# Kernel optimization log

Hardware: AMD Instinct MI355X
Metric: run time of the kernel (lower is better)

The kernel has to match this reference:

```python
import jax, jax.numpy as jnp
import numpy as np

MIN_RES, MAX_RES, NUM_LOD, BAND_WIDTH = 16, 512, 8, 19
CODEBOOK_SIZE = 2 ** BAND_WIDTH  # 524288
_b = np.exp((np.log(MAX_RES) - np.log(MIN_RES)) / (NUM_LOD - 1))
LODS = [int(1 + np.floor(MIN_RES * _b ** l)) for l in range(NUM_LOD)]
SIZES = [min(CODEBOOK_SIZE, r ** 3) for r in LODS]
PRIMES = (1, 2654435761, 805459861)  # Instant-NGP spatial hash primes
N_PTS = 2_000_000

# corner offsets of the unit cube, [8,3]
_OFFS = np.array([[(i >> 2) & 1, (i >> 1) & 1, i & 1] for i in range(8)], dtype=np.int32)


def _hash_interp(p01, table, res, size):
    """Hashed trilinear interpolation for one LOD. p01:[N,3] in [0,1], table:[size]."""
    x = p01 * (res - 1)                                   # [N,3]
    c0 = jnp.clip(jnp.floor(x), 0, res - 2).astype(jnp.int32)
    frac = x - c0.astype(jnp.float32)                     # [N,3]
    offs = jnp.asarray(_OFFS)                             # [8,3]
    corners = (c0[:, None, :] + offs[None]).astype(jnp.uint32)  # [N,8,3]
    h = (corners[..., 0] * jnp.uint32(PRIMES[0])
         ^ corners[..., 1] * jnp.uint32(PRIMES[1])
         ^ corners[..., 2] * jnp.uint32(PRIMES[2]))
    idx = (h % jnp.uint32(size)).astype(jnp.int32)        # [N,8]
    feats = table[idx]                                    # [N,8] gather
    offf = offs.astype(jnp.float32)
    # trilinear weights: prod_d (frac if offset else 1-frac)
    w = jnp.prod(frac[:, None, :] * offf + (1.0 - frac[:, None, :]) * (1.0 - offf), axis=-1)
    return jnp.sum(w * feats, axis=-1)                    # [N]


def setup_inputs() -> dict:
    key = jax.random.key(0)
    k1, k2 = jax.random.split(key)
    pts = jax.random.uniform(k1, (N_PTS, 3), jnp.float32) * 2.0 - 1.0  # [-1,1]^3
    codebook = jax.random.normal(k2, (NUM_LOD, CODEBOOK_SIZE, 1), jnp.float32) * 0.01
    return {"pts": pts, "codebook": codebook}


def reference(pts, codebook):
    p01 = pts / 2.0 + 0.5                                  # normalize to [0,1]
    out = jnp.zeros(pts.shape[0], jnp.float32)
    for i, res in enumerate(LODS):                         # small static loop over LODs
        table = codebook[i, : SIZES[i], 0]                 # static slice -> actual table size
        out = out + _hash_interp(p01, table, res, SIZES[i])
    return out[:, None]                                    # [N, feat_dim=1]
```

## Files before the change

### kernel.cpp

```cpp
#include <hip/hip_runtime.h>
#include <math.h>


static constexpr unsigned CB_STRIDE = 524288u;
static constexpr int WO0 = 0;
static constexpr int WO1 = 4928;
static constexpr int WO2 = 24640;
static constexpr int WO3 = 109824;
static constexpr int WO4 = 467744;
static constexpr int WO5 = 992032;
static constexpr int WO6 = 1516320;
static constexpr int WO7 = 2040608;
static constexpr size_t WS_NEED_BYTES = 2564896u * 2u;

__device__ __forceinline__ unsigned short f32_to_bf16_rne(float f) {
    unsigned u = __float_as_uint(f);
    u = (u + 0x7FFFu + ((u >> 16) & 1u)) >> 16;
    return (unsigned short)u;
}
__device__ __forceinline__ float bf16_to_f32(unsigned short s) {
    return __uint_as_float(((unsigned)s) << 16);
}

template <unsigned SIZE, bool POW2>
__device__ __forceinline__ float lod_interp(float p01x, float p01y, float p01z,
                                            const unsigned short* __restrict__ t,
                                            int res)
{
    const float rm1 = (float)(res - 1);
    float xx = p01x * rm1, yy = p01y * rm1, zz = p01z * rm1;
    const float cmax = (float)(res - 2);
    float fx = fminf(fmaxf(floorf(xx), 0.0f), cmax);
    float fy = fminf(fmaxf(floorf(yy), 0.0f), cmax);
    float fz = fminf(fmaxf(floorf(zz), 0.0f), cmax);
    const float frx = xx - fx, fry = yy - fy, frz = zz - fz;
    const unsigned ix = (unsigned)(int)fx;
    const unsigned iy = (unsigned)(int)fy;
    const unsigned iz = (unsigned)(int)fz;

    const unsigned hx0 = ix;
    const unsigned hx1 = ix + 1u;
    const unsigned hy0 = iy * 2654435761u;
    const unsigned hy1 = hy0 + 2654435761u;
    const unsigned hz0 = iz * 805459861u;
    const unsigned hz1 = hz0 + 805459861u;

    unsigned v0 = hx0 ^ hy0 ^ hz0;
    unsigned v1 = hx0 ^ hy0 ^ hz1;
    unsigned v2 = hx0 ^ hy1 ^ hz0;
    unsigned v3 = hx0 ^ hy1 ^ hz1;
    unsigned v4 = hx1 ^ hy0 ^ hz0;
    unsigned v5 = hx1 ^ hy0 ^ hz1;
    unsigned v6 = hx1 ^ hy1 ^ hz0;
    unsigned v7 = hx1 ^ hy1 ^ hz1;

    if (POW2) {
        const unsigned m = SIZE - 1u;
        v0 &= m; v1 &= m; v2 &= m; v3 &= m; v4 &= m; v5 &= m; v6 &= m; v7 &= m;
    } else {
        v0 %= SIZE; v1 %= SIZE; v2 %= SIZE; v3 %= SIZE;
        v4 %= SIZE; v5 %= SIZE; v6 %= SIZE; v7 %= SIZE;
    }

    const float t000 = bf16_to_f32(t[v0]);
    const float t001 = bf16_to_f32(t[v1]);
    const float t010 = bf16_to_f32(t[v2]);
    const float t011 = bf16_to_f32(t[v3]);
    const float t100 = bf16_to_f32(t[v4]);
    const float t101 = bf16_to_f32(t[v5]);
    const float t110 = bf16_to_f32(t[v6]);
    const float t111 = bf16_to_f32(t[v7]);

    const float wx1 = frx, wx0 = 1.0f - frx;
    const float wy1 = fry, wy0 = 1.0f - fry;
    const float wz1 = frz, wz0 = 1.0f - frz;
    const float w00 = wy0 * wz0, w01 = wy0 * wz1;
    const float w10 = wy1 * wz0, w11 = wy1 * wz1;
    const float sx0 = t000 * w00 + t001 * w01 + t010 * w10 + t011 * w11;
    const float sx1 = t100 * w00 + t101 * w01 + t110 * w10 + t111 * w11;
    return wx0 * sx0 + wx1 * sx1;
}

__global__ __launch_bounds__(1024)
void HashGrid_convert_kernel(const float* __restrict__ codebook,
                             unsigned short* __restrict__ ws)
{
    const int lod = blockIdx.y;
    const int sizes[8] = {4913, 19683, 85184, 357911, 524288, 524288, 524288, 524288};
    const int offs[8]  = {WO0, WO1, WO2, WO3, WO4, WO5, WO6, WO7};
    const int idx = blockIdx.x * 1024 + threadIdx.x;
    if (idx < sizes[lod])
        ws[offs[lod] + idx] = f32_to_bf16_rne(codebook[(unsigned)lod * CB_STRIDE + idx]);
}

__global__ __launch_bounds__(256, 4)
void HashGrid_88278757802387_kernel(const float* __restrict__ pts,
                                    const unsigned short* __restrict__ ws,
                                    float* __restrict__ out,
                                    int n, int res7)
{
    const int i = blockIdx.x * 256 + threadIdx.x;
    if (i >= n) return;

    const float p01x = pts[3 * i + 0] * 0.5f + 0.5f;
    const float p01y = pts[3 * i + 1] * 0.5f + 0.5f;
    const float p01z = pts[3 * i + 2] * 0.5f + 0.5f;

    float acc = 0.0f;
    acc += lod_interp<4913u,   false>(p01x, p01y, p01z, ws + WO0, 17);
    acc += lod_interp<19683u,  false>(p01x, p01y, p01z, ws + WO1, 27);
    acc += lod_interp<85184u,  false>(p01x, p01y, p01z, ws + WO2, 44);
    acc += lod_interp<357911u, false>(p01x, p01y, p01z, ws + WO3, 71);
    acc += lod_interp<524288u, true >(p01x, p01y, p01z, ws + WO4, 116);
    acc += lod_interp<524288u, true >(p01x, p01y, p01z, ws + WO5, 191);
    acc += lod_interp<524288u, true >(p01x, p01y, p01z, ws + WO6, 313);
    acc += lod_interp<524288u, true >(p01x, p01y, p01z, ws + WO7, res7);

    out[i] = acc;
}

__global__ __launch_bounds__(256, 4)
void HashGrid_fallback_kernel(const float* __restrict__ pts,
                              const float* __restrict__ codebook,
                              float* __restrict__ out,
                              int n, int res7)
{
    const int i = blockIdx.x * 256 + threadIdx.x;
    if (i >= n) return;
    const float p01x = pts[3 * i + 0] * 0.5f + 0.5f;
    const float p01y = pts[3 * i + 1] * 0.5f + 0.5f;
    const float p01z = pts[3 * i + 2] * 0.5f + 0.5f;
    float acc = 0.0f;
    const int      reslist[8]  = {17, 27, 44, 71, 116, 191, 313, res7};
    const unsigned sizelist[8] = {4913u, 19683u, 85184u, 357911u, 524288u, 524288u, 524288u, 524288u};
    for (int l = 0; l < 8; ++l) {
        const int res = reslist[l];
        const unsigned size = sizelist[l];
        const float rm1 = (float)(res - 1);
        float xx = p01x * rm1, yy = p01y * rm1, zz = p01z * rm1;
        float fx = fminf(fmaxf(floorf(xx), 0.0f), (float)(res - 2));
        float fy = fminf(fmaxf(floorf(yy), 0.0f), (float)(res - 2));
        float fz = fminf(fmaxf(floorf(zz), 0.0f), (float)(res - 2));
        const float frx = xx - fx, fry = yy - fy, frz = zz - fz;
        const unsigned ix = (unsigned)(int)fx, iy = (unsigned)(int)fy, iz = (unsigned)(int)fz;
        const unsigned hy0 = iy * 2654435761u, hy1 = hy0 + 2654435761u;
        const unsigned hz0 = iz * 805459861u,  hz1 = hz0 + 805459861u;
        const unsigned o0 = (ix ^ hy0 ^ hz0) % size,      o1 = (ix ^ hy0 ^ hz1) % size;
        const unsigned o2 = (ix ^ hy1 ^ hz0) % size,      o3 = (ix ^ hy1 ^ hz1) % size;
        const unsigned o4 = ((ix+1u) ^ hy0 ^ hz0) % size, o5 = ((ix+1u) ^ hy0 ^ hz1) % size;
        const unsigned o6 = ((ix+1u) ^ hy1 ^ hz0) % size, o7 = ((ix+1u) ^ hy1 ^ hz1) % size;
        const float* tab = codebook + (unsigned)l * CB_STRIDE;
        const float wx1 = frx, wx0 = 1.0f - frx;
        const float wy1 = fry, wy0 = 1.0f - fry;
        const float wz1 = frz, wz0 = 1.0f - frz;
        const float w00 = wy0*wz0, w01 = wy0*wz1, w10 = wy1*wz0, w11 = wy1*wz1;
        acc += wx0 * (tab[o0]*w00 + tab[o1]*w01 + tab[o2]*w10 + tab[o3]*w11)
             + wx1 * (tab[o4]*w00 + tab[o5]*w01 + tab[o6]*w10 + tab[o7]*w11);
    }
    out[i] = acc;
}

extern "C" void kernel_launch(void* const* d_in, const int* in_sizes, int n_in,
                              void* d_out, int out_size, void* d_ws, size_t ws_size,
                              hipStream_t stream)
{
    const float* pts      = (const float*)d_in[0];
    const float* codebook = (const float*)d_in[1];
    float* out            = (float*)d_out;
    const int n = in_sizes[0] / 3;

    const double b = exp((log(512.0) - log(16.0)) / 7.0);
    const int res7 = (int)(1.0 + floor(16.0 * pow(b, 7.0)));

    const bool use_ws = (d_ws != nullptr) && (ws_size >= WS_NEED_BYTES);
    const int blocks = (n + 255) / 256;

    if (use_ws) {
        unsigned short* ws = (unsigned short*)d_ws;
        hipLaunchKernelGGL(HashGrid_convert_kernel, dim3(512, 8), dim3(1024),
                           0, stream, codebook, ws);
        hipLaunchKernelGGL(HashGrid_88278757802387_kernel, dim3(blocks), dim3(256),
                           0, stream, pts, ws, out, n, res7);
    } else {
        hipLaunchKernelGGL(HashGrid_fallback_kernel, dim3(blocks), dim3(256),
                           0, stream, pts, codebook, out, n, res7);
    }
}
```

Before: 430.8 us.

## Pipeline hash-table gathers through LDS with global_load_lds and explicit vmcnt waits

Replaces the per-LOD direct gathers with asynchronous global_load_lds dword loads into per-wave LDS slots. Four LODs are kept in flight and consumed with manual s_waitcnt vmcnt counters, issuing the next LOD as each slot drains; bf16 halves are selected from the loaded dword by parity. Point loads and the output store become nontemporal. The aim is to raise memory-level parallelism and hide gather latency, at the cost of 32KB of LDS per block, which may limit occupancy, and fragile hand-counted waits.

```diff
diff --git a/kernel.cpp b/kernel.cpp
--- a/kernel.cpp
+++ b/kernel.cpp
@@ -3,14 +3,14 @@
 
 
 static constexpr unsigned CB_STRIDE = 524288u;
-static constexpr int WO0 = 0;
-static constexpr int WO1 = 4928;
-static constexpr int WO2 = 24640;
-static constexpr int WO3 = 109824;
-static constexpr int WO4 = 467744;
-static constexpr int WO5 = 992032;
-static constexpr int WO6 = 1516320;
-static constexpr int WO7 = 2040608;
+static constexpr unsigned WO0 = 0;
+static constexpr unsigned WO1 = 4928;
+static constexpr unsigned WO2 = 24640;
+static constexpr unsigned WO3 = 109824;
+static constexpr unsigned WO4 = 467744;
+static constexpr unsigned WO5 = 992032;
+static constexpr unsigned WO6 = 1516320;
+static constexpr unsigned WO7 = 2040608;
 static constexpr size_t WS_NEED_BYTES = 2564896u * 2u;
 
 __device__ __forceinline__ unsigned short f32_to_bf16_rne(float f) {
@@ -18,14 +18,29 @@
     u = (u + 0x7FFFu + ((u >> 16) & 1u)) >> 16;
     return (unsigned short)u;
 }
-__device__ __forceinline__ float bf16_to_f32(unsigned short s) {
-    return __uint_as_float(((unsigned)s) << 16);
-}
+
+#define TO_GLB(p) ((const __attribute__((address_space(1))) void*)(p))
+#define TO_LDS(p) ((__attribute__((address_space(3))) void*)(p))
+
+__device__ __forceinline__ void gld(const unsigned short* ws, unsigned elem,
+                                    unsigned* lds_dst)
+{
+    const char* g = (const char*)ws + ((elem * 2u) & ~3u);
+    __builtin_amdgcn_global_load_lds(TO_GLB(g), TO_LDS(lds_dst), 4, 0, 0);
+}
+
+#define VMWAIT(N) do { \
+    asm volatile("s_waitcnt vmcnt(" #N ")" ::: "memory"); \
+    __builtin_amdgcn_sched_barrier(0); \
+} while (0)
+
+struct LodState { unsigned selm; float fx, fy, fz; };
 
 template <unsigned SIZE, bool POW2>
-__device__ __forceinline__ float lod_interp(float p01x, float p01y, float p01z,
-                                            const unsigned short* __restrict__ t,
-                                            int res)
+__device__ __forceinline__ LodState issue_lod(float p01x, float p01y, float p01z,
+                                              int res, unsigned wo,
+                                              const unsigned short* __restrict__ ws,
+                                              unsigned* slot )
 {
     const float rm1 = (float)(res - 1);
     float xx = p01x * rm1, yy = p01y * rm1, zz = p01z * rm1;
@@ -33,7 +48,8 @@
     float fx = fminf(fmaxf(floorf(xx), 0.0f), cmax);
     float fy = fminf(fmaxf(floorf(yy), 0.0f), cmax);
     float fz = fminf(fmaxf(floorf(zz), 0.0f), cmax);
-    const float frx = xx - fx, fry = yy - fy, frz = zz - fz;
+    LodState st;
+    st.fx = xx - fx; st.fy = yy - fy; st.fz = zz - fz;
     const unsigned ix = (unsigned)(int)fx;
     const unsigned iy = (unsigned)(int)fy;
     const unsigned iz = (unsigned)(int)fz;
@@ -62,18 +78,50 @@
         v4 %= SIZE; v5 %= SIZE; v6 %= SIZE; v7 %= SIZE;
     }
 
-    const float t000 = bf16_to_f32(t[v0]);
-    const float t001 = bf16_to_f32(t[v1]);
-    const float t010 = bf16_to_f32(t[v2]);
-    const float t011 = bf16_to_f32(t[v3]);
-    const float t100 = bf16_to_f32(t[v4]);
-    const float t101 = bf16_to_f32(t[v5]);
-    const float t110 = bf16_to_f32(t[v6]);
-    const float t111 = bf16_to_f32(t[v7]);
-
-    const float wx1 = frx, wx0 = 1.0f - frx;
-    const float wy1 = fry, wy0 = 1.0f - fry;
-    const float wz1 = frz, wz0 = 1.0f - frz;
+    st.selm = ((wo + v0) & 1u)        | (((wo + v1) & 1u) << 1)
+            | (((wo + v2) & 1u) << 2) | (((wo + v3) & 1u) << 3)
+            | (((wo + v4) & 1u) << 4) | (((wo + v5) & 1u) << 5)
+            | (((wo + v6) & 1u) << 6) | (((wo + v7) & 1u) << 7);
+
+    gld(ws, wo + v0, slot + 0 * 64);
+    gld(ws, wo + v1, slot + 1 * 64);
+    gld(ws, wo + v2, slot + 2 * 64);
+    gld(ws, wo + v3, slot + 3 * 64);
+    gld(ws, wo + v4, slot + 4 * 64);
+    gld(ws, wo + v5, slot + 5 * 64);
+    gld(ws, wo + v6, slot + 6 * 64);
+    gld(ws, wo + v7, slot + 7 * 64);
+    return st;
+}
+
+__device__ __forceinline__ float pick(unsigned d, unsigned sel) {
+    return __uint_as_float(sel ? (d & 0xffff0000u) : (d << 16));
+}
+
+__device__ __forceinline__ float consume_slot(const unsigned* slot, int lane,
+                                              const LodState& st)
+{
+    const unsigned d0 = slot[0 * 64 + lane];
+    const unsigned d1 = slot[1 * 64 + lane];
+    const unsigned d2 = slot[2 * 64 + lane];
+    const unsigned d3 = slot[3 * 64 + lane];
+    const unsigned d4 = slot[4 * 64 + lane];
+    const unsigned d5 = slot[5 * 64 + lane];
+    const unsigned d6 = slot[6 * 64 + lane];
+    const unsigned d7 = slot[7 * 64 + lane];
+
+    const float t000 = pick(d0, (st.selm >> 0) & 1u);
+    const float t001 = pick(d1, (st.selm >> 1) & 1u);
+    const float t010 = pick(d2, (st.selm >> 2) & 1u);
+    const float t011 = pick(d3, (st.selm >> 3) & 1u);
+    const float t100 = pick(d4, (st.selm >> 4) & 1u);
+    const float t101 = pick(d5, (st.selm >> 5) & 1u);
+    const float t110 = pick(d6, (st.selm >> 6) & 1u);
+    const float t111 = pick(d7, (st.selm >> 7) & 1u);
+
+    const float wx1 = st.fx, wx0 = 1.0f - st.fx;
+    const float wy1 = st.fy, wy0 = 1.0f - st.fy;
+    const float wz1 = st.fz, wz0 = 1.0f - st.fz;
     const float w00 = wy0 * wz0, w01 = wy0 * wz1;
     const float w10 = wy1 * wz0, w11 = wy1 * wz1;
     const float sx0 = t000 * w00 + t001 * w01 + t010 * w10 + t011 * w11;
@@ -87,7 +135,7 @@
 {
     const int lod = blockIdx.y;
     const int sizes[8] = {4913, 19683, 85184, 357911, 524288, 524288, 524288, 524288};
-    const int offs[8]  = {WO0, WO1, WO2, WO3, WO4, WO5, WO6, WO7};
+    const unsigned offs[8] = {WO0, WO1, WO2, WO3, WO4, WO5, WO6, WO7};
     const int idx = blockIdx.x * 1024 + threadIdx.x;
     if (idx < sizes[lod])
         ws[offs[lod] + idx] = f32_to_bf16_rne(codebook[(unsigned)lod * CB_STRIDE + idx]);
@@ -99,24 +147,52 @@
                                     float* __restrict__ out,
                                     int n, int res7)
 {
+    __shared__ unsigned lbuf[4][4][8][64];
+    const int w    = threadIdx.x >> 6;
+    const int lane = threadIdx.x & 63;
+    unsigned* s0 = &lbuf[w][0][0][0];
+    unsigned* s1 = &lbuf[w][1][0][0];
+    unsigned* s2 = &lbuf[w][2][0][0];
+    unsigned* s3 = &lbuf[w][3][0][0];
+
     const int i = blockIdx.x * 256 + threadIdx.x;
     if (i >= n) return;
 
-    const float p01x = pts[3 * i + 0] * 0.5f + 0.5f;
-    const float p01y = pts[3 * i + 1] * 0.5f + 0.5f;
-    const float p01z = pts[3 * i + 2] * 0.5f + 0.5f;
-
-    float acc = 0.0f;
-    acc += lod_interp<4913u,   false>(p01x, p01y, p01z, ws + WO0, 17);
-    acc += lod_interp<19683u,  false>(p01x, p01y, p01z, ws + WO1, 27);
-    acc += lod_interp<85184u,  false>(p01x, p01y, p01z, ws + WO2, 44);
-    acc += lod_interp<357911u, false>(p01x, p01y, p01z, ws + WO3, 71);
-    acc += lod_interp<524288u, true >(p01x, p01y, p01z, ws + WO4, 116);
-    acc += lod_interp<524288u, true >(p01x, p01y, p01z, ws + WO5, 191);
-    acc += lod_interp<524288u, true >(p01x, p01y, p01z, ws + WO6, 313);
-    acc += lod_interp<524288u, true >(p01x, p01y, p01z, ws + WO7, res7);
-
-    out[i] = acc;
+    const float p01x = __builtin_nontemporal_load(pts + 3 * i + 0) * 0.5f + 0.5f;
+    const float p01y = __builtin_nontemporal_load(pts + 3 * i + 1) * 0.5f + 0.5f;
+    const float p01z = __builtin_nontemporal_load(pts + 3 * i + 2) * 0.5f + 0.5f;
+
+    LodState st7 = issue_lod<524288u, true >(p01x, p01y, p01z, res7, WO7, ws, s0);
+    LodState st6 = issue_lod<524288u, true >(p01x, p01y, p01z, 313,  WO6, ws, s1);
+    LodState st5 = issue_lod<524288u, true >(p01x, p01y, p01z, 191,  WO5, ws, s2);
+    LodState st4 = issue_lod<524288u, true >(p01x, p01y, p01z, 116,  WO4, ws, s3);
+
+    VMWAIT(24);
+    float acc = consume_slot(s0, lane, st7);
+    LodState st3 = issue_lod<357911u, false>(p01x, p01y, p01z, 71, WO3, ws, s0);
+
+    VMWAIT(24);
+    acc += consume_slot(s1, lane, st6);
+    LodState st2 = issue_lod<85184u,  false>(p01x, p01y, p01z, 44, WO2, ws, s1);
+
+    VMWAIT(24);
+    acc += consume_slot(s2, lane, st5);
+    LodState st1 = issue_lod<19683u,  false>(p01x, p01y, p01z, 27, WO1, ws, s2);
+
+    VMWAIT(24);
+    acc += consume_slot(s3, lane, st4);
+    LodState st0 = issue_lod<4913u,   false>(p01x, p01y, p01z, 17, WO0, ws, s3);
+
+    VMWAIT(24);
+    acc += consume_slot(s0, lane, st3);
+    VMWAIT(16);
+    acc += consume_slot(s1, lane, st2);
+    VMWAIT(8);
+    acc += consume_slot(s2, lane, st1);
+    VMWAIT(0);
+    acc += consume_slot(s3, lane, st0);
+
+    __builtin_nontemporal_store(acc, out + i);
 }
 
 __global__ __launch_bounds__(256, 4)
```

Result: slower. 463.2 us (+7.5%).
